# Optimization experiments

Hardware: AMD Instinct MI355X
Metric: run time of the kernel (lower is better)

Reference implementation:

```python
import jax, jax.numpy as jnp
from jax import lax
import numpy as np

SEARCH = 9          # search window (asserted == 9 in source)
PAD = SEARCH // 2   # 4
NUM_BINS = 10       # num_dist_bins
BIN_DISP = 0.5      # bin_displacement
NUM_ITER = 3        # num_iter
MIN_FILTER_REG = 1e-5


def _distance_map():
    # DistanceMap: soft-bin the radial distance from the window center.
    c = float(SEARCH // 2)
    yy, xx = jnp.meshgrid(jnp.arange(SEARCH, dtype=jnp.float32),
                          jnp.arange(SEARCH, dtype=jnp.float32), indexing='ij')
    d = jnp.sqrt((yy - c) ** 2 + (xx - c) ** 2) / BIN_DISP          # (9,9)
    k = jnp.arange(NUM_BINS, dtype=jnp.float32)
    bd = d[..., None] - k                                            # (9,9,B)
    vals = jnp.maximum(1.0 - jnp.abs(bd), 0.0)
    last = jnp.clip(bd[..., -1] + 1.0, 0.0, 1.0)                     # saturating last bin
    return vals.at[..., -1].set(last)                                # (9,9,B)


def _local_corr(f, ref_pad, disp):
    # f: (b,c,H,W); ref_pad: (b,c,H+8,W+8) -> scores (b,81,H,W)
    b, c, H, W = f.shape
    def step(_, d):
        r = lax.dynamic_slice(ref_pad, (0, 0, d[0], d[1]), (b, c, H, W))
        return None, jnp.einsum('bchw,bchw->bhw', f, r)
    _, out = lax.scan(step, None, disp)                              # (81,b,H,W)
    return jnp.moveaxis(out, 0, 1)


def _local_corr_t(res, ref_pad, disp):
    # res: (b,81,H,W) -> (b,c,H,W); adjoint of _local_corr w.r.t. the filter arg
    b, c = ref_pad.shape[0], ref_pad.shape[1]
    H, W = res.shape[2], res.shape[3]
    def step(acc, xs):
        d, rd = xs                                                   # rd: (b,H,W)
        r = lax.dynamic_slice(ref_pad, (0, 0, d[0], d[1]), (b, c, H, W))
        return acc + rd[:, None] * r, None
    acc0 = jnp.zeros((b, c, H, W), ref_pad.dtype)
    acc, _ = lax.scan(step, acc0, (disp, jnp.moveaxis(res, 1, 0)))
    return acc


def setup_inputs() -> dict:
    key = jax.random.key(0)
    k1, k2 = jax.random.split(key)
    b, c, H, W = 4, 128, 128, 128
    d = jnp.arange(NUM_BINS, dtype=jnp.float32) * BIN_DISP
    return {
        'filter_map': jax.random.normal(k1, (b, c, H, W), jnp.float32),
        'reference_feat': jax.random.normal(k2, (b, c, H, W), jnp.float32),
        # 1x1-conv predictor weights (num_bins -> 1), at their documented inits:
        'label_w': jnp.exp(-0.5 * d ** 2),            # init_gauss, sigma=1.0
        'spatial_w': jnp.ones((NUM_BINS,), jnp.float32),
        'mask_w': 4.0 * jnp.tanh(2.0 - d),            # v_minus_init_factor * tanh(2 - d)
        'log_step_length': jnp.zeros((1,), jnp.float32),   # log(1.0)
        'filter_reg': 0.01 * jnp.ones((1,), jnp.float32),
    }


def reference(filter_map, reference_feat, label_w, spatial_w, mask_w,
              log_step_length, filter_reg):
    b, c, H, W = filter_map.shape
    dm = _distance_map()                                             # (9,9,B)
    target_map = (dm @ label_w).reshape(1, SEARCH * SEARCH, 1, 1)
    v_plus = (dm @ spatial_w).reshape(1, SEARCH * SEARCH, 1, 1)
    weight_m = jax.nn.sigmoid(dm @ mask_w).reshape(1, SEARCH * SEARCH, 1, 1)

    step_length = jnp.exp(log_step_length).reshape(1, 1, 1, 1)
    reg_weight = jnp.maximum(filter_reg * filter_reg,
                             MIN_FILTER_REG ** 2).reshape(1, 1, 1, 1) / (c * c)

    dys, dxs = jnp.meshgrid(jnp.arange(SEARCH), jnp.arange(SEARCH), indexing='ij')
    disp = jnp.stack([dys.ravel(), dxs.ravel()], axis=1)             # (81,2)
    ref_pad = jnp.pad(reference_feat, ((0, 0), (0, 0), (PAD, PAD), (PAD, PAD)))

    # LeakyReluPar: f(s,a) = (1-a)/2*|s| + (1+a)/2*s ; deriv: (1-a)/2*sign(s) + (1+a)/2
    a_lo = (1.0 - weight_m) * 0.5
    a_hi = (1.0 + weight_m) * 0.5

    f = filter_map
    for _ in range(NUM_ITER):
        scores = _local_corr(f, ref_pad, disp)                       # (b,81,H,W)
        act = v_plus * (a_lo * jnp.abs(scores) + a_hi * scores)
        grad_act = v_plus * (a_lo * jnp.sign(scores) + a_hi)
        residuals = act - v_plus * target_map
        mapped = grad_act * residuals
        f_grad = reg_weight * f + _local_corr_t(mapped, ref_pad, disp)
        sg = grad_act * _local_corr(f_grad, ref_pad, disp)
        alpha_den = jnp.sum(sg * sg, axis=1, keepdims=True)          # (b,1,H,W)
        alpha_num = jnp.sum(f_grad * f_grad, axis=1, keepdims=True)
        alpha = alpha_num / jnp.maximum(alpha_den + reg_weight * alpha_num, 1e-8)
        f = f - step_length * alpha * f_grad
    return f
```

## Files before the change

### kernel.cpp

```cpp
#include <hip/hip_runtime.h>

#define BB 4
#define CC 128
#define HH 128
#define WW 128
#define HW (HH*WW)
#define CHW (CC*HW)
#define ND 81
#define CP 136
#define UPITCH 40
#define PP 40

typedef short s8v __attribute__((ext_vector_type(8)));
typedef short s4v __attribute__((ext_vector_type(4)));
typedef float f4v __attribute__((ext_vector_type(4)));

__device__ __forceinline__ short f2bf(float x){
  unsigned u = __float_as_uint(x);
  unsigned r = (u + 0x7FFFu + ((u >> 16) & 1u)) >> 16;
  return (short)r;
}
__device__ __forceinline__ float bf2f(short s){
  return __uint_as_float(((unsigned)(unsigned short)s) << 16);
}

__global__ void coef_kernel(const float* lw, const float* sw, const float* mw,
                            const float* lsl, const float* fr, float* coef){
  int d = threadIdx.x;
  if (d < ND){
    float dy = (float)(d / 9) - 4.0f;
    float dx = (float)(d % 9) - 4.0f;
    float dist = sqrtf(dy*dy + dx*dx) * 2.0f;
    float t = 0.f, v = 0.f, m = 0.f;
    for (int k = 0; k < 10; k++){
      float bd = dist - (float)k;
      float val = (k == 9) ? fminf(fmaxf(bd + 1.0f, 0.f), 1.f)
                           : fmaxf(1.0f - fabsf(bd), 0.f);
      t += val * lw[k]; v += val * sw[k]; m += val * mw[k];
    }
    float wm = 1.f / (1.f + expf(-m));
    float ah = (1.f + wm) * 0.5f;
    float gp = v, gn = v * wm, gz = v * ah;
    float vt = v * t;
    coef[(d*3+0)*2+0] = gp * gp;  coef[(d*3+0)*2+1] = gp * vt;
    coef[(d*3+1)*2+0] = gn * gn;  coef[(d*3+1)*2+1] = gn * vt;
    coef[(d*3+2)*2+0] = gz * gz;  coef[(d*3+2)*2+1] = gz * vt;
  }
  if (threadIdx.x == 0){
    coef[500] = expf(lsl[0]);
    float f = fr[0];
    coef[501] = fmaxf(f*f, 1e-10f) / (float)(CC*CC);
  }
}

__global__ __launch_bounds__(256)
void cvt_kernel(const float* ref, short* refT, short* refU){
  __shared__ short T[128*130];
  int r = blockIdx.x, bb = blockIdx.y;
  int tid = threadIdx.x;
  const float* src = ref + (size_t)bb*CHW + (size_t)r*WW;
  short* uout = refU + (size_t)(bb*HH + r) * CC * WW;
  short* tout = refT + (size_t)(bb*HH + r) * WW * CC;
  #pragma unroll
  for (int k = 0; k < 16; k++){
    int q = tid + (k << 8);
    int c = q >> 5, u0 = (q & 31) * 4;
    float4 v = *(const float4*)(src + (size_t)c*HW + u0);
    short h0 = f2bf(v.x), h1 = f2bf(v.y), h2 = f2bf(v.z), h3 = f2bf(v.w);
    s4v pk = {h0, h1, h2, h3};
    *(s4v*)&uout[(size_t)c*WW + u0] = pk;
    T[c*130 + u0 + 0] = h0; T[c*130 + u0 + 1] = h1;
    T[c*130 + u0 + 2] = h2; T[c*130 + u0 + 3] = h3;
  }
  __syncthreads();
  #pragma unroll
  for (int k = 0; k < 16; k++){
    int o = tid + (k << 8);
    int u = o >> 5, c0 = (o & 31) * 4;
    s4v pk = {T[(c0+0)*130 + u], T[(c0+1)*130 + u],
              T[(c0+2)*130 + u], T[(c0+3)*130 + u]};
    *(s4v*)&tout[(size_t)u*CC + c0] = pk;
  }
}

#define L_UC   0
#define L_FGS  8704
#define L_CU   8704
#define L_PM   18944
#define L_CF   26112
#define L_DEN  28160
#define L_NUM  28416
#define L_SA   28672
#define L_SZ   28928

template<int PRE>
__global__ __launch_bounds__(256, 4)
void kF(const float* f_in, const float* ref, const short* refT, const short* refU,
        const float* coef, float* f_out){
  __shared__ char smem[L_SZ];
  short* uc  = (short*)(smem + L_UC);
  short* cu  = (short*)(smem + L_CU);
  short* Pm  = (short*)(smem + L_PM);
  short* fgs = (short*)(smem + L_FGS);
  float* s_cf = (float*)(smem + L_CF);
  float* den = (float*)(smem + L_DEN);
  float* num = (float*)(smem + L_NUM);
  float* sa  = (float*)(smem + L_SA);

  int tid = threadIdx.x;
  int lane = tid & 63, wv = tid >> 6;
  int quad = lane >> 4, col = lane & 15;

  int hwid = blockIdx.x + (blockIdx.y << 3) + (blockIdx.z << 8);
  int virt = ((hwid & 7) << 7) + (hwid >> 3);
  int bb = virt >> 8, y0 = ((virt >> 3) & 31) * 4, x0 = (virt & 7) * 16;

  int ub = x0 - 8;

  const float* fimg = f_in + (size_t)bb * CHW;
  const float* rimg = ref  + (size_t)bb * CHW;

  s8v pT0, pT1, pU0, pU1;
  float4 pF0, pF1, pF2, pF3;

  auto loadT = [&](int r){
    if constexpr (PRE){
      const short* tb = refT + (size_t)(bb*HH + r) * WW * CC;
      { int e = tid;       int ua = ub + (e >> 4);
        pT0 = (ua >= 0 && ua < WW)
              ? *(const s8v*)(tb + (size_t)ua*CC + ((e & 15) << 3)) : (s8v)(short)0; }
      { int e = tid + 256; int ua = ub + (e >> 4);
        pT1 = (ua >= 0 && ua < WW)
              ? *(const s8v*)(tb + (size_t)ua*CC + ((e & 15) << 3)) : (s8v)(short)0; }
    } else {
      const float* rb = rimg + (size_t)r * WW;
      float4 z; z.x = z.y = z.z = z.w = 0.f;
      { int e = tid;       int ua = ub + (e & 7)*4;
        pF0 = (ua >= 0 && ua + 4 <= WW) ? *(const float4*)(rb + (size_t)(e >> 3)*HW + ua) : z; }
      { int e = tid + 256; int ua = ub + (e & 7)*4;
        pF1 = (ua >= 0 && ua + 4 <= WW) ? *(const float4*)(rb + (size_t)(e >> 3)*HW + ua) : z; }
      { int e = tid + 512; int ua = ub + (e & 7)*4;
        pF2 = (ua >= 0 && ua + 4 <= WW) ? *(const float4*)(rb + (size_t)(e >> 3)*HW + ua) : z; }
      { int e = tid + 768; int ua = ub + (e & 7)*4;
        pF3 = (ua >= 0 && ua + 4 <= WW) ? *(const float4*)(rb + (size_t)(e >> 3)*HW + ua) : z; }
    }
  };
  auto loadU = [&](int r){
    if constexpr (PRE){
      const short* ubp = refU + (size_t)(bb*HH + r) * CC * WW;
      { int e = tid;       int ua = ub + ((e & 3) << 3);
        pU0 = (ua >= 0 && ua + 8 <= WW)
              ? *(const s8v*)(ubp + (size_t)(e >> 2)*WW + ua) : (s8v)(short)0; }
      { int e = tid + 256; int ua = ub + ((e & 3) << 3);
        pU1 = (ua >= 0 && ua + 8 <= WW)
              ? *(const s8v*)(ubp + (size_t)(e >> 2)*WW + ua) : (s8v)(short)0; }
    }
  };
  auto writeRowA = [&](){
    if constexpr (PRE){
      { int e = tid;       *(s8v*)&uc[(e >> 4)*CP + ((e & 15) << 3)] = pT0; }
      { int e = tid + 256; *(s8v*)&uc[(e >> 4)*CP + ((e & 15) << 3)] = pT1; }
      { int e = tid;       *(s8v*)&cu[(e >> 2)*UPITCH + ((e & 3) << 3)] = pU0; }
      { int e = tid + 256; *(s8v*)&cu[(e >> 2)*UPITCH + ((e & 3) << 3)] = pU1; }
    } else {
      float4 vv[4] = {pF0, pF1, pF2, pF3};
      #pragma unroll
      for (int k = 0; k < 4; k++){
        int e4 = tid + (k << 8);
        int u4 = (e4 & 7) * 4, c = e4 >> 3;
        short h0 = f2bf(vv[k].x), h1 = f2bf(vv[k].y),
              h2 = f2bf(vv[k].z), h3 = f2bf(vv[k].w);
        uc[(u4+0)*CP + c] = h0; uc[(u4+1)*CP + c] = h1;
        uc[(u4+2)*CP + c] = h2; uc[(u4+3)*CP + c] = h3;
        s4v pk = {h0, h1, h2, h3};
        *(s4v*)&cu[c*UPITCH + u4] = pk;
      }
    }
  };
  auto writeRowB = [&](){
    if constexpr (PRE){
      { int e = tid;       *(s8v*)&uc[(e >> 4)*CP + ((e & 15) << 3)] = pT0; }
      { int e = tid + 256; *(s8v*)&uc[(e >> 4)*CP + ((e & 15) << 3)] = pT1; }
    } else {
      float4 vv[4] = {pF0, pF1, pF2, pF3};
      #pragma unroll
      for (int k = 0; k < 4; k++){
        int e4 = tid + (k << 8);
        int u4 = (e4 & 7) * 4, c = e4 >> 3;
        uc[(u4+0)*CP + c] = f2bf(vv[k].x); uc[(u4+1)*CP + c] = f2bf(vv[k].y);
        uc[(u4+2)*CP + c] = f2bf(vv[k].z); uc[(u4+3)*CP + c] = f2bf(vv[k].w);
      }
    }
  };

  if (y0 - 4 >= 0){ loadT(y0 - 4); loadU(y0 - 4); }

  for (int e = tid; e < 512; e += 256) s_cf[e] = coef[e];

  int fy = y0 + wv;
  s8v a_hi[4], a_lo[4];
  #pragma unroll
  for (int kc = 0; kc < 4; kc++){
    short th[8], tl[8];
    #pragma unroll
    for (int j = 0; j < 8; j++){
      int c = kc*32 + quad*8 + j;
      float v = fimg[(size_t)c * HW + fy * WW + x0 + col];
      short h = f2bf(v);
      th[j] = h; tl[j] = f2bf(v - bf2f(h));
    }
    a_hi[kc] = *(const s8v*)th;
    a_lo[kc] = *(const s8v*)tl;
  }

  f4v D[8];
  #pragma unroll
  for (int i = 0; i < 8; i++) D[i] = (f4v)0.f;

  unsigned long long f0 = 0ull, f1 = 0ull, f2 = 0ull;

  for (int rr = 0; rr < 12; rr++){
    int r = y0 + rr - 4;
    bool rv = (r >= 0) && (r < HH);
    __syncthreads();
    if (rv) writeRowA();
    __syncthreads();
    if (rr < 11){
      int rn = r + 1;
      if (rn >= 0 && rn < HH){ loadT(rn); loadU(rn); }
    }
    int dy = rr - wv;
    if (dy >= 0 && dy <= 8){
      unsigned pack = 0u;
      if (rv){
        f4v C0 = (f4v)0.f, C1 = (f4v)0.f;
        #pragma unroll
        for (int kc = 0; kc < 4; kc++){
          s8v b0 = *(const s8v*)&uc[col*CP      + kc*32 + quad*8];
          s8v b1 = *(const s8v*)&uc[(16+col)*CP + kc*32 + quad*8];
          C0 = __builtin_amdgcn_mfma_f32_16x16x32_bf16(a_hi[kc], b0, C0, 0,0,0);
          C0 = __builtin_amdgcn_mfma_f32_16x16x32_bf16(a_lo[kc], b0, C0, 0,0,0);
          C1 = __builtin_amdgcn_mfma_f32_16x16x32_bf16(a_hi[kc], b1, C1, 0,0,0);
          C1 = __builtin_amdgcn_mfma_f32_16x16x32_bf16(a_lo[kc], b1, C1, 0,0,0);
        }
        #pragma unroll
        for (int nt = 0; nt < 2; nt++){
          f4v Cv = nt ? C1 : C0;
          #pragma unroll
          for (int reg = 0; reg < 4; reg++){
            int x  = quad*4 + reg;
            int up = nt*16 + col;
            int dxm = up - x - 4;
            float m = 0.f;
            if ((unsigned)dxm <= 8u){
              float s = Cv[reg];
              int d = dy*9 + dxm;
              unsigned pos = (s > 0.f) ? 1u : 0u;
              unsigned neg = (s < 0.f) ? 1u : 0u;
              int cse = pos ? 0 : (neg ? 1 : 2);
              float2 gg = *(const float2*)&s_cf[(d*3 + cse)*2];
              m = fmaf(gg.x, s, -gg.y);
              pack |= (pos | (neg << 1)) << ((nt*4 + reg) * 2);
            }
            Pm[(wv*16 + x)*PP + up] = f2bf(m);
          }
        }
        asm volatile("s_waitcnt lgkmcnt(0)" ::: "memory");
        __builtin_amdgcn_sched_barrier(0);
        s8v pa = *(const s8v*)&Pm[(wv*16 + col)*PP + quad*8];
        #pragma unroll
        for (int ct = 0; ct < 8; ct++){
          s8v bc = *(const s8v*)&cu[(ct*16 + col)*UPITCH + quad*8];
          D[ct] = __builtin_amdgcn_mfma_f32_16x16x32_bf16(pa, bc, D[ct], 0,0,0);
        }
      }
      f0 = (f0 >> 16) | (f1 << 48);
      f1 = (f1 >> 16) | (f2 << 48);
      f2 = (f2 >> 16) | ((unsigned long long)pack << 48);
    }
  }

  if (y0 - 4 >= 0) loadT(y0 - 4);

  float rw = s_cf[501];
  __syncthreads();
  #pragma unroll
  for (int ct = 0; ct < 8; ct++){
    #pragma unroll
    for (int reg = 0; reg < 4; reg++){
      int x = quad*4 + reg, c = ct*16 + col;
      float fv = fimg[(size_t)c * HW + fy * WW + x0 + x];
      fgs[(wv*16 + x)*CP + c] = f2bf(D[ct][reg] + rw * fv);
    }
  }
  __syncthreads();
  if (tid < 64){
    float s = 0.f;
    #pragma unroll
    for (int kc = 0; kc < 16; kc++){
      s8v v = *(const s8v*)&fgs[tid*CP + kc*8];
      #pragma unroll
      for (int j = 0; j < 8; j++){ float f = bf2f(v[j]); s += f*f; }
    }
    num[tid] = s;
  }

  s8v ga_[4];
  #pragma unroll
  for (int kc = 0; kc < 4; kc++)
    ga_[kc] = *(const s8v*)&fgs[(wv*16 + col)*CP + kc*32 + quad*8];

  float dacc[4] = {0.f, 0.f, 0.f, 0.f};

  for (int rr = 0; rr < 12; rr++){
    int r = y0 + rr - 4;
    bool rv = (r >= 0) && (r < HH);
    __syncthreads();
    if (rv) writeRowB();
    __syncthreads();
    if (rr < 11){
      int rn = r + 1;
      if (rn >= 0 && rn < HH) loadT(rn);
    }
    int dy = rr - wv;
    if (dy >= 0 && dy <= 8){
      unsigned pack = (unsigned)(f0 >> 48) & 0xFFFFu;
      f0 = (f0 >> 16) | (f1 << 48);
      f1 = (f1 >> 16) | (f2 << 48);
      f2 >>= 16;
      if (rv){
        f4v C0 = (f4v)0.f, C1 = (f4v)0.f;
        #pragma unroll
        for (int kc = 0; kc < 4; kc++){
          s8v b0 = *(const s8v*)&uc[col*CP      + kc*32 + quad*8];
          s8v b1 = *(const s8v*)&uc[(16+col)*CP + kc*32 + quad*8];
          C0 = __builtin_amdgcn_mfma_f32_16x16x32_bf16(ga_[kc], b0, C0, 0,0,0);
          C1 = __builtin_amdgcn_mfma_f32_16x16x32_bf16(ga_[kc], b1, C1, 0,0,0);
        }
        #pragma unroll
        for (int nt = 0; nt < 2; nt++){
          f4v Cv = nt ? C1 : C0;
          #pragma unroll
          for (int reg = 0; reg < 4; reg++){
            int x  = quad*4 + reg;
            int up = nt*16 + col;
            int dxm = up - x - 4;
            if ((unsigned)dxm <= 8u){
              int d = dy*9 + dxm;
              unsigned b2 = pack >> ((nt*4 + reg) * 2);
              int cse = (b2 & 1u) ? 0 : ((b2 & 2u) ? 1 : 2);
              float g2 = s_cf[(d*3 + cse)*2];
              float t  = Cv[reg];
              dacc[reg] = fmaf(g2 * t, t, dacc[reg]);
            }
          }
        }
      }
    }
  }

  #pragma unroll
  for (int reg = 0; reg < 4; reg++){
    float v = dacc[reg];
    v += __shfl_xor(v, 1);
    v += __shfl_xor(v, 2);
    v += __shfl_xor(v, 4);
    v += __shfl_xor(v, 8);
    if (col == 0) den[wv*16 + quad*4 + reg] = v;
  }

  __syncthreads();
  if (tid < 64){
    float step = s_cf[500];
    float alpha = num[tid] / fmaxf(den[tid] + rw*num[tid], 1e-8f);
    sa[tid] = step * alpha;
  }
  __syncthreads();

  float* oimg = f_out + (size_t)bb * CHW;
  for (int e = tid; e < 8192; e += 256){
    int x = e & 15, y = (e >> 4) & 3, c = e >> 6;
    size_t gi = (size_t)c * HW + (y0 + y) * WW + x0 + x;
    float v = fimg[gi] - sa[y*16 + x] * bf2f(fgs[(y*16 + x)*CP + c]);
    oimg[gi] = v;
  }
}

extern "C" void kernel_launch(void* const* d_in, const int* in_sizes, int n_in,
                              void* d_out, int out_size, void* d_ws, size_t ws_size,
                              hipStream_t stream) {
  const float* filter_map = (const float*)d_in[0];
  const float* ref        = (const float*)d_in[1];
  const float* label_w    = (const float*)d_in[2];
  const float* spatial_w  = (const float*)d_in[3];
  const float* mask_w     = (const float*)d_in[4];
  const float* lsl        = (const float*)d_in[5];
  const float* freg       = (const float*)d_in[6];

  float* coef = (float*)d_ws;
  float* fbuf = (float*)d_out;

  short* refT = (short*)((char*)d_ws + 65536);
  short* refU = refT + (size_t)BB * CHW;
  size_t need = 65536 + 2 * (size_t)BB * CHW * sizeof(short);
  bool pre = (ws_size >= need);

  coef_kernel<<<dim3(1), dim3(128), 0, stream>>>(label_w, spatial_w, mask_w, lsl, freg, coef);
  if (pre)
    cvt_kernel<<<dim3(HH, BB), dim3(256), 0, stream>>>(ref, refT, refU);

  dim3 grid(8, 32, BB);
  for (int it = 0; it < 3; it++){
    const float* fsrc = (it == 0) ? filter_map : (const float*)fbuf;
    if (pre) kF<1><<<grid, 256, 0, stream>>>(fsrc, ref, refT, refU, coef, fbuf);
    else     kF<0><<<grid, 256, 0, stream>>>(fsrc, ref, refT, refU, coef, fbuf);
  }
}
```

Measured before the change: 334.7 us.

## Load reference tiles directly from global memory into MFMA operands, drop LDS staging

Removes the per-row shared-memory staging of the reference row (uc/cu buffers) and the two block-wide barriers per row. Each wave now loops over its own 9 displacement rows and loads MFMA B operands straight from the pre-transposed bf16 global arrays, with a fast path for interior tiles. This removes synchronisation and LDS traffic and shrinks shared memory. In exchange, neighbouring waves re-read the same rows from global/L2 memory instead of sharing them, and the non-PRE path falls back to scalar strided global loads.

New measurement: 467.2 us. 1.4x slower.

```diff
diff --git a/kernel.cpp b/kernel.cpp
--- a/kernel.cpp
+++ b/kernel.cpp
@@ -8,7 +8,6 @@
 #define CHW (CC*HW)
 #define ND 81
 #define CP 136
-#define UPITCH 40
 #define PP 40
 
 typedef short s8v __attribute__((ext_vector_type(8)));
@@ -83,23 +82,19 @@
   }
 }
 
-#define L_UC   0
-#define L_FGS  8704
-#define L_CU   8704
-#define L_PM   18944
-#define L_CF   26112
-#define L_DEN  28160
-#define L_NUM  28416
-#define L_SA   28672
-#define L_SZ   28928
+#define L_PM   0
+#define L_FGS  5120
+#define L_CF   22528
+#define L_DEN  24576
+#define L_NUM  24832
+#define L_SA   25088
+#define L_SZ   25344
 
 template<int PRE>
 __global__ __launch_bounds__(256, 4)
 void kF(const float* f_in, const float* ref, const short* refT, const short* refU,
         const float* coef, float* f_out){
   __shared__ char smem[L_SZ];
-  short* uc  = (short*)(smem + L_UC);
-  short* cu  = (short*)(smem + L_CU);
   short* Pm  = (short*)(smem + L_PM);
   short* fgs = (short*)(smem + L_FGS);
   float* s_cf = (float*)(smem + L_CF);
@@ -116,84 +111,12 @@
   int bb = virt >> 8, y0 = ((virt >> 3) & 31) * 4, x0 = (virt & 7) * 16;
 
   int ub = x0 - 8;
+  bool interior = (ub >= 0) && (ub + 32 <= WW);
 
   const float* fimg = f_in + (size_t)bb * CHW;
   const float* rimg = ref  + (size_t)bb * CHW;
-
-  s8v pT0, pT1, pU0, pU1;
-  float4 pF0, pF1, pF2, pF3;
-
-  auto loadT = [&](int r){
-    if constexpr (PRE){
-      const short* tb = refT + (size_t)(bb*HH + r) * WW * CC;
-      { int e = tid;       int ua = ub + (e >> 4);
-        pT0 = (ua >= 0 && ua < WW)
-              ? *(const s8v*)(tb + (size_t)ua*CC + ((e & 15) << 3)) : (s8v)(short)0; }
-      { int e = tid + 256; int ua = ub + (e >> 4);
-        pT1 = (ua >= 0 && ua < WW)
-              ? *(const s8v*)(tb + (size_t)ua*CC + ((e & 15) << 3)) : (s8v)(short)0; }
-    } else {
-      const float* rb = rimg + (size_t)r * WW;
-      float4 z; z.x = z.y = z.z = z.w = 0.f;
-      { int e = tid;       int ua = ub + (e & 7)*4;
-        pF0 = (ua >= 0 && ua + 4 <= WW) ? *(const float4*)(rb + (size_t)(e >> 3)*HW + ua) : z; }
-      { int e = tid + 256; int ua = ub + (e & 7)*4;
-        pF1 = (ua >= 0 && ua + 4 <= WW) ? *(const float4*)(rb + (size_t)(e >> 3)*HW + ua) : z; }
-      { int e = tid + 512; int ua = ub + (e & 7)*4;
-        pF2 = (ua >= 0 && ua + 4 <= WW) ? *(const float4*)(rb + (size_t)(e >> 3)*HW + ua) : z; }
-      { int e = tid + 768; int ua = ub + (e & 7)*4;
-        pF3 = (ua >= 0 && ua + 4 <= WW) ? *(const float4*)(rb + (size_t)(e >> 3)*HW + ua) : z; }
-    }
-  };
-  auto loadU = [&](int r){
-    if constexpr (PRE){
-      const short* ubp = refU + (size_t)(bb*HH + r) * CC * WW;
-      { int e = tid;       int ua = ub + ((e & 3) << 3);
-        pU0 = (ua >= 0 && ua + 8 <= WW)
-              ? *(const s8v*)(ubp + (size_t)(e >> 2)*WW + ua) : (s8v)(short)0; }
-      { int e = tid + 256; int ua = ub + ((e & 3) << 3);
-        pU1 = (ua >= 0 && ua + 8 <= WW)
-              ? *(const s8v*)(ubp + (size_t)(e >> 2)*WW + ua) : (s8v)(short)0; }
-    }
-  };
-  auto writeRowA = [&](){
-    if constexpr (PRE){
-      { int e = tid;       *(s8v*)&uc[(e >> 4)*CP + ((e & 15) << 3)] = pT0; }
-      { int e = tid + 256; *(s8v*)&uc[(e >> 4)*CP + ((e & 15) << 3)] = pT1; }
-      { int e = tid;       *(s8v*)&cu[(e >> 2)*UPITCH + ((e & 3) << 3)] = pU0; }
-      { int e = tid + 256; *(s8v*)&cu[(e >> 2)*UPITCH + ((e & 3) << 3)] = pU1; }
-    } else {
-      float4 vv[4] = {pF0, pF1, pF2, pF3};
-      #pragma unroll
-      for (int k = 0; k < 4; k++){
-        int e4 = tid + (k << 8);
-        int u4 = (e4 & 7) * 4, c = e4 >> 3;
-        short h0 = f2bf(vv[k].x), h1 = f2bf(vv[k].y),
-              h2 = f2bf(vv[k].z), h3 = f2bf(vv[k].w);
-        uc[(u4+0)*CP + c] = h0; uc[(u4+1)*CP + c] = h1;
-        uc[(u4+2)*CP + c] = h2; uc[(u4+3)*CP + c] = h3;
-        s4v pk = {h0, h1, h2, h3};
-        *(s4v*)&cu[c*UPITCH + u4] = pk;
-      }
-    }
-  };
-  auto writeRowB = [&](){
-    if constexpr (PRE){
-      { int e = tid;       *(s8v*)&uc[(e >> 4)*CP + ((e & 15) << 3)] = pT0; }
-      { int e = tid + 256; *(s8v*)&uc[(e >> 4)*CP + ((e & 15) << 3)] = pT1; }
-    } else {
-      float4 vv[4] = {pF0, pF1, pF2, pF3};
-      #pragma unroll
-      for (int k = 0; k < 4; k++){
-        int e4 = tid + (k << 8);
-        int u4 = (e4 & 7) * 4, c = e4 >> 3;
-        uc[(u4+0)*CP + c] = f2bf(vv[k].x); uc[(u4+1)*CP + c] = f2bf(vv[k].y);
-        uc[(u4+2)*CP + c] = f2bf(vv[k].z); uc[(u4+3)*CP + c] = f2bf(vv[k].w);
-      }
-    }
-  };
-
-  if (y0 - 4 >= 0){ loadT(y0 - 4); loadU(y0 - 4); }
+  const short* tb  = refT + (size_t)bb * HH * WW * CC;
+  const short* ubp = refU + (size_t)bb * HH * CC * WW;
 
   for (int e = tid; e < 512; e += 256) s_cf[e] = coef[e];
 
@@ -213,77 +136,107 @@
     a_lo[kc] = *(const s8v*)tl;
   }
 
+  __syncthreads();
+
+  float rw = s_cf[501];
+
   f4v D[8];
   #pragma unroll
   for (int i = 0; i < 8; i++) D[i] = (f4v)0.f;
 
   unsigned long long f0 = 0ull, f1 = 0ull, f2 = 0ull;
 
-  for (int rr = 0; rr < 12; rr++){
-    int r = y0 + rr - 4;
-    bool rv = (r >= 0) && (r < HH);
-    __syncthreads();
-    if (rv) writeRowA();
-    __syncthreads();
-    if (rr < 11){
-      int rn = r + 1;
-      if (rn >= 0 && rn < HH){ loadT(rn); loadU(rn); }
-    }
-    int dy = rr - wv;
-    if (dy >= 0 && dy <= 8){
-      unsigned pack = 0u;
-      if (rv){
-        f4v C0 = (f4v)0.f, C1 = (f4v)0.f;
+  for (int dy = 0; dy <= 8; ++dy){
+    int r = fy - 4 + dy;
+    unsigned pack = 0u;
+    if (r >= 0 && r < HH){
+      const short* trow = tb  + (size_t)r * WW * CC;
+      const short* urow = ubp + (size_t)r * CC * WW;
+      f4v C0 = (f4v)0.f, C1 = (f4v)0.f;
+      #pragma unroll
+      for (int kc = 0; kc < 4; kc++){
+        s8v b0, b1;
+        if constexpr (PRE){
+          if (interior){
+            b0 = *(const s8v*)(trow + (ub +      col)*CC + kc*32 + quad*8);
+            b1 = *(const s8v*)(trow + (ub + 16 + col)*CC + kc*32 + quad*8);
+          } else {
+            int ua0 = ub + col, ua1 = ub + 16 + col;
+            b0 = (ua0 >= 0 && ua0 < WW)
+                 ? *(const s8v*)(trow + ua0*CC + kc*32 + quad*8) : (s8v)(short)0;
+            b1 = (ua1 >= 0 && ua1 < WW)
+                 ? *(const s8v*)(trow + ua1*CC + kc*32 + quad*8) : (s8v)(short)0;
+          }
+        } else {
+          short t0[8], t1[8];
+          int ua0 = ub + col, ua1 = ub + 16 + col;
+          #pragma unroll
+          for (int j = 0; j < 8; j++){
+            int c = kc*32 + quad*8 + j;
+            t0[j] = (ua0 >= 0 && ua0 < WW) ? f2bf(rimg[(size_t)c*HW + r*WW + ua0]) : (short)0;
+            t1[j] = (ua1 >= 0 && ua1 < WW) ? f2bf(rimg[(size_t)c*HW + r*WW + ua1]) : (short)0;
+          }
+          b0 = *(const s8v*)t0; b1 = *(const s8v*)t1;
+        }
+        C0 = __builtin_amdgcn_mfma_f32_16x16x32_bf16(a_hi[kc], b0, C0, 0,0,0);
+        C0 = __builtin_amdgcn_mfma_f32_16x16x32_bf16(a_lo[kc], b0, C0, 0,0,0);
+        C1 = __builtin_amdgcn_mfma_f32_16x16x32_bf16(a_hi[kc], b1, C1, 0,0,0);
+        C1 = __builtin_amdgcn_mfma_f32_16x16x32_bf16(a_lo[kc], b1, C1, 0,0,0);
+      }
+      #pragma unroll
+      for (int nt = 0; nt < 2; nt++){
+        f4v Cv = nt ? C1 : C0;
         #pragma unroll
-        for (int kc = 0; kc < 4; kc++){
-          s8v b0 = *(const s8v*)&uc[col*CP      + kc*32 + quad*8];
-          s8v b1 = *(const s8v*)&uc[(16+col)*CP + kc*32 + quad*8];
-          C0 = __builtin_amdgcn_mfma_f32_16x16x32_bf16(a_hi[kc], b0, C0, 0,0,0);
-          C0 = __builtin_amdgcn_mfma_f32_16x16x32_bf16(a_lo[kc], b0, C0, 0,0,0);
-          C1 = __builtin_amdgcn_mfma_f32_16x16x32_bf16(a_hi[kc], b1, C1, 0,0,0);
-          C1 = __builtin_amdgcn_mfma_f32_16x16x32_bf16(a_lo[kc], b1, C1, 0,0,0);
-        }
-        #pragma unroll
-        for (int nt = 0; nt < 2; nt++){
-          f4v Cv = nt ? C1 : C0;
+        for (int reg = 0; reg < 4; reg++){
+          int x  = quad*4 + reg;
+          int up = nt*16 + col;
+          int dxm = up - x - 4;
+          float m = 0.f;
+          if ((unsigned)dxm <= 8u){
+            float s = Cv[reg];
+            int d = dy*9 + dxm;
+            unsigned pos = (s > 0.f) ? 1u : 0u;
+            unsigned neg = (s < 0.f) ? 1u : 0u;
+            int cse = pos ? 0 : (neg ? 1 : 2);
+            float2 gg = *(const float2*)&s_cf[(d*3 + cse)*2];
+            m = fmaf(gg.x, s, -gg.y);
+            pack |= (pos | (neg << 1)) << ((nt*4 + reg) * 2);
+          }
+          Pm[(wv*16 + x)*PP + up] = f2bf(m);
+        }
+      }
+      asm volatile("s_waitcnt lgkmcnt(0)" ::: "memory");
+      __builtin_amdgcn_sched_barrier(0);
+      s8v pa = *(const s8v*)&Pm[(wv*16 + col)*PP + quad*8];
+      #pragma unroll
+      for (int ct = 0; ct < 8; ct++){
+        s8v bc;
+        if constexpr (PRE){
+          if (interior){
+            bc = *(const s8v*)(urow + (size_t)(ct*16 + col)*WW + ub + quad*8);
+          } else {
+            int ua = ub + quad*8;
+            bc = (ua >= 0 && ua + 8 <= WW)
+                 ? *(const s8v*)(urow + (size_t)(ct*16 + col)*WW + ua) : (s8v)(short)0;
+          }
+        } else {
+          short t0[8];
+          int c = ct*16 + col;
           #pragma unroll
-          for (int reg = 0; reg < 4; reg++){
-            int x  = quad*4 + reg;
-            int up = nt*16 + col;
-            int dxm = up - x - 4;
-            float m = 0.f;
-            if ((unsigned)dxm <= 8u){
-              float s = Cv[reg];
-              int d = dy*9 + dxm;
-              unsigned pos = (s > 0.f) ? 1u : 0u;
-              unsigned neg = (s < 0.f) ? 1u : 0u;
-              int cse = pos ? 0 : (neg ? 1 : 2);
-              float2 gg = *(const float2*)&s_cf[(d*3 + cse)*2];
-              m = fmaf(gg.x, s, -gg.y);
-              pack |= (pos | (neg << 1)) << ((nt*4 + reg) * 2);
-            }
-            Pm[(wv*16 + x)*PP + up] = f2bf(m);
-          }
-        }
-        asm volatile("s_waitcnt lgkmcnt(0)" ::: "memory");
-        __builtin_amdgcn_sched_barrier(0);
-        s8v pa = *(const s8v*)&Pm[(wv*16 + col)*PP + quad*8];
-        #pragma unroll
-        for (int ct = 0; ct < 8; ct++){
-          s8v bc = *(const s8v*)&cu[(ct*16 + col)*UPITCH + quad*8];
-          D[ct] = __builtin_amdgcn_mfma_f32_16x16x32_bf16(pa, bc, D[ct], 0,0,0);
-        }
-      }
-      f0 = (f0 >> 16) | (f1 << 48);
-      f1 = (f1 >> 16) | (f2 << 48);
-      f2 = (f2 >> 16) | ((unsigned long long)pack << 48);
-    }
-  }
-
-  if (y0 - 4 >= 0) loadT(y0 - 4);
-
-  float rw = s_cf[501];
-  __syncthreads();
+          for (int j = 0; j < 8; j++){
+            int ua = ub + quad*8 + j;
+            t0[j] = (ua >= 0 && ua < WW) ? f2bf(rimg[(size_t)c*HW + r*WW + ua]) : (short)0;
+          }
+          bc = *(const s8v*)t0;
+        }
+        D[ct] = __builtin_amdgcn_mfma_f32_16x16x32_bf16(pa, bc, D[ct], 0,0,0);
+      }
+    }
+    f0 = (f0 >> 16) | (f1 << 48);
+    f1 = (f1 >> 16) | (f2 << 48);
+    f2 = (f2 >> 16) | ((unsigned long long)pack << 48);
+  }
+
   #pragma unroll
   for (int ct = 0; ct < 8; ct++){
     #pragma unroll
@@ -312,47 +265,58 @@
 
   float dacc[4] = {0.f, 0.f, 0.f, 0.f};
 
-  for (int rr = 0; rr < 12; rr++){
-    int r = y0 + rr - 4;
-    bool rv = (r >= 0) && (r < HH);
-    __syncthreads();
-    if (rv) writeRowB();
-    __syncthreads();
-    if (rr < 11){
-      int rn = r + 1;
-      if (rn >= 0 && rn < HH) loadT(rn);
-    }
-    int dy = rr - wv;
-    if (dy >= 0 && dy <= 8){
-      unsigned pack = (unsigned)(f0 >> 48) & 0xFFFFu;
-      f0 = (f0 >> 16) | (f1 << 48);
-      f1 = (f1 >> 16) | (f2 << 48);
-      f2 >>= 16;
-      if (rv){
-        f4v C0 = (f4v)0.f, C1 = (f4v)0.f;
+  for (int dy = 0; dy <= 8; ++dy){
+    int r = fy - 4 + dy;
+    unsigned pack = (unsigned)(f0 >> 48) & 0xFFFFu;
+    f0 = (f0 >> 16) | (f1 << 48);
+    f1 = (f1 >> 16) | (f2 << 48);
+    f2 >>= 16;
+    if (r >= 0 && r < HH){
+      const short* trow = tb + (size_t)r * WW * CC;
+      f4v C0 = (f4v)0.f, C1 = (f4v)0.f;
+      #pragma unroll
+      for (int kc = 0; kc < 4; kc++){
+        s8v b0, b1;
+        if constexpr (PRE){
+          if (interior){
+            b0 = *(const s8v*)(trow + (ub +      col)*CC + kc*32 + quad*8);
+            b1 = *(const s8v*)(trow + (ub + 16 + col)*CC + kc*32 + quad*8);
+          } else {
+            int ua0 = ub + col, ua1 = ub + 16 + col;
+            b0 = (ua0 >= 0 && ua0 < WW)
+                 ? *(const s8v*)(trow + ua0*CC + kc*32 + quad*8) : (s8v)(short)0;
+            b1 = (ua1 >= 0 && ua1 < WW)
+                 ? *(const s8v*)(trow + ua1*CC + kc*32 + quad*8) : (s8v)(short)0;
+          }
+        } else {
+          short t0[8], t1[8];
+          int ua0 = ub + col, ua1 = ub + 16 + col;
+          #pragma unroll
+          for (int j = 0; j < 8; j++){
+            int c = kc*32 + quad*8 + j;
+            t0[j] = (ua0 >= 0 && ua0 < WW) ? f2bf(rimg[(size_t)c*HW + r*WW + ua0]) : (short)0;
+            t1[j] = (ua1 >= 0 && ua1 < WW) ? f2bf(rimg[(size_t)c*HW + r*WW + ua1]) : (short)0;
+          }
+          b0 = *(const s8v*)t0; b1 = *(const s8v*)t1;
+        }
+        C0 = __builtin_amdgcn_mfma_f32_16x16x32_bf16(ga_[kc], b0, C0, 0,0,0);
+        C1 = __builtin_amdgcn_mfma_f32_16x16x32_bf16(ga_[kc], b1, C1, 0,0,0);
+      }
+      #pragma unroll
+      for (int nt = 0; nt < 2; nt++){
+        f4v Cv = nt ? C1 : C0;
         #pragma unroll
-        for (int kc = 0; kc < 4; kc++){
-          s8v b0 = *(const s8v*)&uc[col*CP      + kc*32 + quad*8];
-          s8v b1 = *(const s8v*)&uc[(16+col)*CP + kc*32 + quad*8];
-          C0 = __builtin_amdgcn_mfma_f32_16x16x32_bf16(ga_[kc], b0, C0, 0,0,0);
-          C1 = __builtin_amdgcn_mfma_f32_16x16x32_bf16(ga_[kc], b1, C1, 0,0,0);
-        }
-        #pragma unroll
-        for (int nt = 0; nt < 2; nt++){
-          f4v Cv = nt ? C1 : C0;
-          #pragma unroll
-          for (int reg = 0; reg < 4; reg++){
-            int x  = quad*4 + reg;
-            int up = nt*16 + col;
-            int dxm = up - x - 4;
-            if ((unsigned)dxm <= 8u){
-              int d = dy*9 + dxm;
-              unsigned b2 = pack >> ((nt*4 + reg) * 2);
-              int cse = (b2 & 1u) ? 0 : ((b2 & 2u) ? 1 : 2);
-              float g2 = s_cf[(d*3 + cse)*2];
-              float t  = Cv[reg];
-              dacc[reg] = fmaf(g2 * t, t, dacc[reg]);
-            }
+        for (int reg = 0; reg < 4; reg++){
+          int x  = quad*4 + reg;
+          int up = nt*16 + col;
+          int dxm = up - x - 4;
+          if ((unsigned)dxm <= 8u){
+            int d = dy*9 + dxm;
+            unsigned b2 = pack >> ((nt*4 + reg) * 2);
+            int cse = (b2 & 1u) ? 0 : ((b2 & 2u) ? 1 : 2);
+            float g2 = s_cf[(d*3 + cse)*2];
+            float t  = Cv[reg];
+            dacc[reg] = fmaf(g2 * t, t, dacc[reg]);
           }
         }
       }
```
